# Performance work log

Measured on AMD Instinct MI355X. Metric: run time of the kernel, lower is better.

Reference implementation:

```python
import jax, jax.numpy as jnp
import numpy as np

N_NODES = 50000
N_EDGES = 800000
IN_C, HID_C, OUT_C = 64, 64, 32


def setup_inputs() -> dict:
    key = jax.random.key(0)
    ks = jax.random.split(key, 8)
    x = jax.random.normal(ks[0], (N_NODES, IN_C), dtype=jnp.float32)
    edge_index = jax.random.randint(ks[1], (2, N_EDGES), 0, N_NODES, dtype=jnp.int64)
    s1 = 1.0 / np.sqrt(IN_C)
    s2 = 1.0 / np.sqrt(HID_C)
    W_rel1 = jax.random.uniform(ks[2], (IN_C, HID_C), jnp.float32, -s1, s1)
    W_root1 = jax.random.uniform(ks[3], (IN_C, HID_C), jnp.float32, -s1, s1)
    b1 = jax.random.uniform(ks[4], (HID_C,), jnp.float32, -s1, s1)
    W_rel2 = jax.random.uniform(ks[5], (HID_C, OUT_C), jnp.float32, -s2, s2)
    W_root2 = jax.random.uniform(ks[6], (HID_C, OUT_C), jnp.float32, -s2, s2)
    b2 = jax.random.uniform(ks[7], (OUT_C,), jnp.float32, -s2, s2)
    return {"x": x, "edge_index": edge_index, "W_rel1": W_rel1, "W_root1": W_root1,
            "b1": b1, "W_rel2": W_rel2, "W_root2": W_root2, "b2": b2}


def _graph_conv(x, src, dst, W_rel, W_root, b):
    # aggregate neighbor features (sum over incoming edges), then linear
    agg = jax.ops.segment_sum(x[src], dst, num_segments=N_NODES)  # [N, C_in]
    return agg @ W_rel + x @ W_root + b


def reference(x, edge_index, W_rel1, W_root1, b1, W_rel2, W_root2, b2):
    src, dst = edge_index[0], edge_index[1]
    h = jax.nn.relu(_graph_conv(x, src, dst, W_rel1, W_root1, b1))
    out = _graph_conv(h, src, dst, W_rel2, W_root2, b2)
    return out
```

## Files before the change

kernel.cpp:

```cpp
#include <hip/hip_runtime.h>

static constexpr int N_NODES = 50000;
static constexpr int N_EDGES = 800000;

static constexpr int NBK      = 196;
static constexpr int BCAP     = 5120;
static constexpr int MAXE     = BCAP / 512;
static constexpr int BIN_TILE = 4096;
static constexpr int BIN_BLOCKS = (N_EDGES + BIN_TILE - 1) / BIN_TILE;
static constexpr int PRE1_TILES  = (N_NODES + 15) / 16;
static constexpr int PRE1_BLOCKS = (PRE1_TILES + 3) / 4;

typedef __attribute__((ext_vector_type(8))) short   bf16x8;
typedef __attribute__((ext_vector_type(4))) float   floatx4;

__device__ __forceinline__ unsigned short f2b(float f) {
    union { float f; unsigned u; } v; v.f = f;
    unsigned r = v.u + 0x7FFFu + ((v.u >> 16) & 1u);
    return (unsigned short)(r >> 16);
}
__device__ __forceinline__ float blo(unsigned v) {
    union { unsigned u; float f; } c; c.u = v << 16; return c.f;
}
__device__ __forceinline__ float bhi(unsigned v) {
    union { unsigned u; float f; } c; c.u = v & 0xffff0000u; return c.f;
}
__device__ __forceinline__ unsigned pk2(float a, float b) {
    return (unsigned)f2b(a) | ((unsigned)f2b(b) << 16);
}

__device__ __forceinline__ void bin_body(
    int bb, const int* __restrict__ srcv, const int* __restrict__ dstv,
    int* __restrict__ bcnt, unsigned* __restrict__ epair)
{
    __shared__ unsigned stage[BIN_TILE];
    __shared__ int cnt[256];
    __shared__ int scn[256];
    __shared__ int wtot[4], wbase[4];
    __shared__ int pref[NBK];
    __shared__ int gbase[NBK];

    int tid   = threadIdx.x;
    int lane  = tid & 63;
    int wv    = tid >> 6;
    int base  = bb * BIN_TILE;
    int tileN = min(BIN_TILE, N_EDGES - base);

    cnt[tid] = 0;
    __syncthreads();

    unsigned pk[16]; int sl[16];
#pragma unroll
    for (int j = 0; j < 16; ++j) {
        int i = tid + j * 256;
        pk[j] = 0xFFFFFFFFu; sl[j] = 0;
        if (i < tileN) {
            unsigned s = (unsigned)srcv[base + i];
            unsigned d = (unsigned)dstv[base + i];
            pk[j] = (s << 16) | d;
            sl[j] = atomicAdd(&cnt[d >> 8], 1);
        }
    }
    __syncthreads();

    {
        int v = cnt[tid];
        int orig = v;
        for (int off = 1; off < 64; off <<= 1) {
            int t2 = __shfl_up(v, off);
            if (lane >= off) v += t2;
        }
        scn[tid] = v - orig;
        if (lane == 63) wtot[wv] = v;
    }
    __syncthreads();
    if (tid == 0) {
        int r = 0;
#pragma unroll
        for (int k = 0; k < 4; ++k) { int t2 = wtot[k]; wbase[k] = r; r += t2; }
    }
    __syncthreads();
    if (tid < NBK) {
        pref[tid]  = scn[tid] + wbase[wv];
        gbase[tid] = tid * BCAP + atomicAdd(&bcnt[tid], cnt[tid]);
    }
    __syncthreads();

#pragma unroll
    for (int j = 0; j < 16; ++j) {
        if (pk[j] != 0xFFFFFFFFu) {
            int b = (int)((pk[j] & 0xFFFFu) >> 8);
            stage[pref[b] + sl[j]] = pk[j];
        }
    }
    __syncthreads();

    for (int i = tid; i < tileN; i += 256) {
        unsigned pd = stage[i];
        int b = (int)((pd & 0xFFFFu) >> 8);
        epair[(size_t)gbase[b] + (i - pref[b])] = ((pd >> 16) << 8) | (pd & 255u);
    }
}

__device__ __forceinline__ void pre1_body(
    int bb, const float* __restrict__ x,
    const float* __restrict__ Wrel, const float* __restrict__ Wroot,
    const float* __restrict__ bias,
    unsigned short* __restrict__ u1, unsigned short* __restrict__ r1)
{
    int lane = threadIdx.x & 63;
    int c15  = lane & 15;
    int q    = lane >> 4;

    bf16x8 bf[2][4][2];
#pragma unroll
    for (int mat = 0; mat < 2; ++mat) {
        const float* W = mat ? Wroot : Wrel;
#pragma unroll
        for (int ct = 0; ct < 4; ++ct) {
            int c = ct * 16 + c15;
#pragma unroll
            for (int kf = 0; kf < 2; ++kf) {
                int kb = kf * 32 + q * 8;
                bf16x8 f;
#pragma unroll
                for (int j = 0; j < 8; ++j)
                    f[j] = (short)f2b(W[(kb + j) * 64 + c]);
                bf[mat][ct][kf] = f;
            }
        }
    }
    float bv[4];
#pragma unroll
    for (int ct = 0; ct < 4; ++ct) bv[ct] = bias[ct * 16 + c15];

    int tile = bb * 4 + (threadIdx.x >> 6);
    if (tile * 16 >= N_NODES) return;
    int row0 = tile * 16;

    const float* xr = x + (size_t)(row0 + c15) * 64;
    bf16x8 a0, a1;
#pragma unroll
    for (int j = 0; j < 8; ++j) {
        a0[j] = (short)f2b(xr[q * 8 + j]);
        a1[j] = (short)f2b(xr[32 + q * 8 + j]);
    }

    floatx4 z = {0.f, 0.f, 0.f, 0.f};
    floatx4 acc[2][4];
#pragma unroll
    for (int mat = 0; mat < 2; ++mat)
#pragma unroll
        for (int ct = 0; ct < 4; ++ct) {
            floatx4 a = __builtin_amdgcn_mfma_f32_16x16x32_bf16(a0, bf[mat][ct][0], z, 0, 0, 0);
            acc[mat][ct] = __builtin_amdgcn_mfma_f32_16x16x32_bf16(a1, bf[mat][ct][1], a, 0, 0, 0);
        }

#pragma unroll
    for (int reg = 0; reg < 4; ++reg) {
        int row = row0 + q * 4 + reg;
        uint2 uu, rr;
        uu.x = pk2(acc[0][0][reg],          acc[0][1][reg]);
        uu.y = pk2(acc[0][2][reg],          acc[0][3][reg]);
        rr.x = pk2(acc[1][0][reg] + bv[0],  acc[1][1][reg] + bv[1]);
        rr.y = pk2(acc[1][2][reg] + bv[2],  acc[1][3][reg] + bv[3]);
        *reinterpret_cast<uint2*>(u1 + (size_t)row * 64 + c15 * 4) = uu;
        *reinterpret_cast<uint2*>(r1 + (size_t)row * 64 + c15 * 4) = rr;
    }
}

__global__ __launch_bounds__(256) void k_binpre1(
    const int* __restrict__ srcv, const int* __restrict__ dstv,
    int* __restrict__ bcnt, unsigned* __restrict__ epair,
    const float* __restrict__ x,
    const float* __restrict__ Wrel, const float* __restrict__ Wroot,
    const float* __restrict__ bias,
    unsigned short* __restrict__ u1, unsigned short* __restrict__ r1)
{
    if ((int)blockIdx.x < BIN_BLOCKS)
        bin_body(blockIdx.x, srcv, dstv, bcnt, epair);
    else
        pre1_body(blockIdx.x - BIN_BLOCKS, x, Wrel, Wroot, bias, u1, r1);
}

__global__ __launch_bounds__(512) void k_build(
    const unsigned* __restrict__ epair, const int* __restrict__ bcnt,
    int* __restrict__ offsets, int* __restrict__ esrc)
{
    __shared__ int cnt[256];
    __shared__ int scn[256];
    __shared__ int start[256];
    __shared__ int wtot[4], wbase[4];
    __shared__ int s_base;

    int b = blockIdx.x;
    int t = threadIdx.x;
    int lane = t & 63;
    int node0 = b << 8;
    int ncnt  = min(256, N_NODES - node0);
    int beg   = b * BCAP;
    int m     = bcnt[b];

    if (t < 256) cnt[t] = 0;
    __syncthreads();

    unsigned ev[MAXE]; int sl[MAXE];
#pragma unroll
    for (int j = 0; j < MAXE; ++j) {
        int i = t + j * 512;
        ev[j] = 0; sl[j] = -1;
        if (i < m) {
            ev[j] = epair[beg + i];
            sl[j] = atomicAdd(&cnt[ev[j] & 255u], 1);
        }
    }

    if (t < 64) {
        int pre = 0;
#pragma unroll
        for (int k = 0; k < 4; ++k) {
            int i = t + (k << 6);
            if (i < b) pre += bcnt[i];
        }
        for (int off = 1; off < 64; off <<= 1) pre += __shfl_xor(pre, off);
        if (t == 0) s_base = pre;
    }
    __syncthreads();

    if (t < 256) {
        int v = cnt[t];
        int orig = v;
        for (int off = 1; off < 64; off <<= 1) {
            int t2 = __shfl_up(v, off);
            if (lane >= off) v += t2;
        }
        scn[t] = v - orig;
        if (lane == 63) wtot[t >> 6] = v;
    }
    __syncthreads();
    if (t == 0) {
        int r = 0;
#pragma unroll
        for (int k = 0; k < 4; ++k) { int q = wtot[k]; wbase[k] = r; r += q; }
    }
    __syncthreads();
    if (t < 256) {
        int st = s_base + scn[t] + wbase[t >> 6];
        start[t] = st;
        if (t < ncnt) offsets[node0 + t] = st;
    }
    if (b == 0 && t == 0) offsets[N_NODES] = N_EDGES;
    __syncthreads();

#pragma unroll
    for (int j = 0; j < MAXE; ++j) {
        if (sl[j] >= 0)
            esrc[start[ev[j] & 255u] + sl[j]] = (int)(ev[j] >> 8);
    }
}

__global__ __launch_bounds__(1024) void k_aggf(
    const unsigned short* __restrict__ u1,
    const unsigned short* __restrict__ r1,
    const int* __restrict__ offsets, const int* __restrict__ esrc,
    const float* __restrict__ Wrel,
    const float* __restrict__ Wroot,
    const float* __restrict__ bias,
    unsigned short* __restrict__ u2,
    unsigned short* __restrict__ r2)
{
    __shared__ unsigned short hlds[16 * 64];

    int w    = threadIdx.x >> 6;
    int lane = threadIdx.x & 63;
    int j    = lane & 7;
    int slot = lane >> 3;

    int node = blockIdx.x * 16 + w;
    if (node < N_NODES) {
        int beg = offsets[node], end = offsets[node + 1];
        float s0 = 0.f, s1 = 0.f, s2 = 0.f, s3 = 0.f;
        float s4 = 0.f, s5 = 0.f, s6 = 0.f, s7 = 0.f;
        for (int e = beg + slot; e < end; e += 8) {
            int sv = esrc[e];
            uint4 v = *reinterpret_cast<const uint4*>(u1 + (size_t)sv * 64 + j * 8);
            s0 += blo(v.x); s1 += bhi(v.x);
            s2 += blo(v.y); s3 += bhi(v.y);
            s4 += blo(v.z); s5 += bhi(v.z);
            s6 += blo(v.w); s7 += bhi(v.w);
        }
        s0 += __shfl_xor(s0, 32); s1 += __shfl_xor(s1, 32);
        s2 += __shfl_xor(s2, 32); s3 += __shfl_xor(s3, 32);
        s4 += __shfl_xor(s4, 32); s5 += __shfl_xor(s5, 32);
        s6 += __shfl_xor(s6, 32); s7 += __shfl_xor(s7, 32);
        s0 += __shfl_xor(s0, 16); s1 += __shfl_xor(s1, 16);
        s2 += __shfl_xor(s2, 16); s3 += __shfl_xor(s3, 16);
        s4 += __shfl_xor(s4, 16); s5 += __shfl_xor(s5, 16);
        s6 += __shfl_xor(s6, 16); s7 += __shfl_xor(s7, 16);
        s0 += __shfl_xor(s0, 8);  s1 += __shfl_xor(s1, 8);
        s2 += __shfl_xor(s2, 8);  s3 += __shfl_xor(s3, 8);
        s4 += __shfl_xor(s4, 8);  s5 += __shfl_xor(s5, 8);
        s6 += __shfl_xor(s6, 8);  s7 += __shfl_xor(s7, 8);
        if (lane < 8) {
            uint4 rv = *reinterpret_cast<const uint4*>(r1 + (size_t)node * 64 + j * 8);
            float v0 = fmaxf(s0 + blo(rv.x), 0.f);
            float v1 = fmaxf(s1 + bhi(rv.x), 0.f);
            float v2 = fmaxf(s2 + blo(rv.y), 0.f);
            float v3 = fmaxf(s3 + bhi(rv.y), 0.f);
            float v4 = fmaxf(s4 + blo(rv.z), 0.f);
            float v5 = fmaxf(s5 + bhi(rv.z), 0.f);
            float v6 = fmaxf(s6 + blo(rv.w), 0.f);
            float v7 = fmaxf(s7 + bhi(rv.w), 0.f);
            uint4 o;
            o.x = pk2(v0, v1); o.y = pk2(v2, v3);
            o.z = pk2(v4, v5); o.w = pk2(v6, v7);
            unsigned byte = (unsigned)w * 128u + (((unsigned)j * 16u) ^ (((unsigned)w & 7u) << 4));
            *reinterpret_cast<uint4*>((char*)hlds + byte) = o;
        }
    }
    __syncthreads();

    if (w >= 2) return;
    int row0 = blockIdx.x * 16;
    if (row0 >= N_NODES) return;
    int c15 = lane & 15;
    int q   = lane >> 4;

    const float* W = w ? Wroot : Wrel;
    bf16x8 bf[2][2];
#pragma unroll
    for (int ct = 0; ct < 2; ++ct) {
        int c = ct * 16 + c15;
#pragma unroll
        for (int kf = 0; kf < 2; ++kf) {
            bf16x8 f;
#pragma unroll
            for (int jj = 0; jj < 8; ++jj) {
                int p = kf * 32 + q * 8 + jj;
                int tk = (p & 3) * 16 + (p >> 2);
                f[jj] = (short)f2b(W[tk * 32 + c]);
            }
            bf[ct][kf] = f;
        }
    }
    float bv[2];
#pragma unroll
    for (int ct = 0; ct < 2; ++ct) bv[ct] = w ? bias[ct * 16 + c15] : 0.0f;

    int r = c15;
    unsigned sw = ((unsigned)r & 7u) << 4;
    bf16x8 a0 = *reinterpret_cast<const bf16x8*>((char*)hlds + (unsigned)r * 128u + (((unsigned)q * 16u) ^ sw));
    bf16x8 a1 = *reinterpret_cast<const bf16x8*>((char*)hlds + (unsigned)r * 128u + ((((unsigned)q + 4u) * 16u) ^ sw));

    floatx4 z = {0.f, 0.f, 0.f, 0.f};
    floatx4 acc[2];
#pragma unroll
    for (int ct = 0; ct < 2; ++ct) {
        floatx4 a = __builtin_amdgcn_mfma_f32_16x16x32_bf16(a0, bf[ct][0], z, 0, 0, 0);
        acc[ct] = __builtin_amdgcn_mfma_f32_16x16x32_bf16(a1, bf[ct][1], a, 0, 0, 0);
    }

    unsigned short* dst = w ? r2 : u2;
#pragma unroll
    for (int reg = 0; reg < 4; ++reg) {
        int row = row0 + q * 4 + reg;
        unsigned vv = pk2(acc[0][reg] + bv[0], acc[1][reg] + bv[1]);
        *reinterpret_cast<unsigned*>(dst + (size_t)row * 32 + c15 * 2) = vv;
    }
}

__global__ __launch_bounds__(256) void k_agg32(
    const unsigned short* __restrict__ u2,
    const unsigned short* __restrict__ r2,
    const int* __restrict__ offsets, const int* __restrict__ esrc,
    float* __restrict__ out)
{
    int lane = threadIdx.x & 63;
    int node = (blockIdx.x * blockDim.x + threadIdx.x) >> 6;
    if (node >= N_NODES) return;
    int j    = lane & 3;
    int slot = lane >> 2;
    int beg = offsets[node], end = offsets[node + 1];
    float s0 = 0.f, s1 = 0.f, s2 = 0.f, s3 = 0.f;
    float s4 = 0.f, s5 = 0.f, s6 = 0.f, s7 = 0.f;
    for (int e = beg + slot; e < end; e += 16) {
        int sv = esrc[e];
        uint4 v = *reinterpret_cast<const uint4*>(u2 + (size_t)sv * 32 + j * 8);
        s0 += blo(v.x); s1 += bhi(v.x);
        s2 += blo(v.y); s3 += bhi(v.y);
        s4 += blo(v.z); s5 += bhi(v.z);
        s6 += blo(v.w); s7 += bhi(v.w);
    }
    s0 += __shfl_xor(s0, 32); s1 += __shfl_xor(s1, 32);
    s2 += __shfl_xor(s2, 32); s3 += __shfl_xor(s3, 32);
    s4 += __shfl_xor(s4, 32); s5 += __shfl_xor(s5, 32);
    s6 += __shfl_xor(s6, 32); s7 += __shfl_xor(s7, 32);
    s0 += __shfl_xor(s0, 16); s1 += __shfl_xor(s1, 16);
    s2 += __shfl_xor(s2, 16); s3 += __shfl_xor(s3, 16);
    s4 += __shfl_xor(s4, 16); s5 += __shfl_xor(s5, 16);
    s6 += __shfl_xor(s6, 16); s7 += __shfl_xor(s7, 16);
    s0 += __shfl_xor(s0, 8);  s1 += __shfl_xor(s1, 8);
    s2 += __shfl_xor(s2, 8);  s3 += __shfl_xor(s3, 8);
    s4 += __shfl_xor(s4, 8);  s5 += __shfl_xor(s5, 8);
    s6 += __shfl_xor(s6, 8);  s7 += __shfl_xor(s7, 8);
    s0 += __shfl_xor(s0, 4);  s1 += __shfl_xor(s1, 4);
    s2 += __shfl_xor(s2, 4);  s3 += __shfl_xor(s3, 4);
    s4 += __shfl_xor(s4, 4);  s5 += __shfl_xor(s5, 4);
    s6 += __shfl_xor(s6, 4);  s7 += __shfl_xor(s7, 4);
    if (lane < 4) {
        uint4 rv = *reinterpret_cast<const uint4*>(r2 + (size_t)node * 32 + j * 8);
        float4 oA, oB;
        oA.x = s0 + blo(rv.x);  oB.x = s1 + bhi(rv.x);
        oA.y = s2 + blo(rv.y);  oB.y = s3 + bhi(rv.y);
        oA.z = s4 + blo(rv.z);  oB.z = s5 + bhi(rv.z);
        oA.w = s6 + blo(rv.w);  oB.w = s7 + bhi(rv.w);
        *reinterpret_cast<float4*>(out + (size_t)node * 32 + j * 4)      = oA;
        *reinterpret_cast<float4*>(out + (size_t)node * 32 + 16 + j * 4) = oB;
    }
}

extern "C" void kernel_launch(void* const* d_in, const int* in_sizes, int n_in,
                              void* d_out, int out_size, void* d_ws, size_t ws_size,
                              hipStream_t stream) {
    const float* x      = (const float*)d_in[0];
    const int*   ei     = (const int*)  d_in[1];
    const float* Wrel1  = (const float*)d_in[2];
    const float* Wroot1 = (const float*)d_in[3];
    const float* b1     = (const float*)d_in[4];
    const float* Wrel2  = (const float*)d_in[5];
    const float* Wroot2 = (const float*)d_in[6];
    const float* b2     = (const float*)d_in[7];
    float*       out    = (float*)d_out;

    const int* srcv = ei;
    const int* dstv = ei + N_EDGES;

    char* p = (char*)d_ws;
    auto alloc = [&](size_t bytes) {
        char* r = p;
        p += (bytes + 255) & ~(size_t)255;
        return r;
    };
    int*      offsets = (int*)     alloc(sizeof(int) * (N_NODES + 1));
    int*      bcnt    = (int*)     alloc(sizeof(int) * NBK);
    unsigned* epair   = (unsigned*)alloc(sizeof(unsigned) * (size_t)NBK * BCAP);
    int*      esrc    = (int*)     alloc(sizeof(int) * N_EDGES);
    unsigned short* u1 = (unsigned short*)alloc(sizeof(short) * (size_t)N_NODES * 64);
    unsigned short* r1 = (unsigned short*)alloc(sizeof(short) * (size_t)N_NODES * 64);
    unsigned short* u2 = (unsigned short*)alloc(sizeof(short) * (size_t)N_NODES * 32);
    unsigned short* r2 = (unsigned short*)alloc(sizeof(short) * (size_t)N_NODES * 32);

    const int nodeBlocks = (N_NODES * 64 + 255) / 256;
    const int aggfBlocks = (N_NODES + 15) / 16;

    hipMemsetAsync(bcnt, 0, sizeof(int) * NBK, stream);
    k_binpre1<<<BIN_BLOCKS + PRE1_BLOCKS, 256, 0, stream>>>(
        srcv, dstv, bcnt, epair, x, Wrel1, Wroot1, b1, u1, r1);
    k_build<<<NBK, 512, 0, stream>>>(epair, bcnt, offsets, esrc);

    k_aggf<<<aggfBlocks, 1024, 0, stream>>>(u1, r1, offsets, esrc,
                                            Wrel2, Wroot2, b2, u2, r2);

    k_agg32<<<nodeBlocks, 256, 0, stream>>>(u2, r2, offsets, esrc, out);
}
```

Before: 86.45 us.

## Split layer-1 dense transform across bin and build kernels to balance load

Splits the layer-1 node-transform blocks (MFMA x·W) into two halves: one still fused with edge binning, the other fused into the CSR build kernel. The build kernel now runs with 256 threads per block instead of 512, holding twice as many edges per thread in registers. The aim is to fill idle CUs during the small build launch and shorten the binning launch. In exchange, the build phase carries more register pressure per thread and longer serial loops.

```diff
diff --git a/kernel.cpp b/kernel.cpp
--- a/kernel.cpp
+++ b/kernel.cpp
@@ -5,11 +5,12 @@
 
 static constexpr int NBK      = 196;
 static constexpr int BCAP     = 5120;
-static constexpr int MAXE     = BCAP / 512;
+static constexpr int MAXE     = BCAP / 256;
 static constexpr int BIN_TILE = 4096;
 static constexpr int BIN_BLOCKS = (N_EDGES + BIN_TILE - 1) / BIN_TILE;
-static constexpr int PRE1_TILES  = (N_NODES + 15) / 16;
-static constexpr int PRE1_BLOCKS = (PRE1_TILES + 3) / 4;
+static constexpr int PRE1_TILES = (N_NODES + 15) / 16;
+static constexpr int PRE1_SPLIT = 391;
+static constexpr int PRE1_REST  = 391;
 
 typedef __attribute__((ext_vector_type(8))) short   bf16x8;
 typedef __attribute__((ext_vector_type(4))) float   floatx4;
@@ -103,7 +104,7 @@
 }
 
 __device__ __forceinline__ void pre1_body(
-    int bb, const float* __restrict__ x,
+    int tile, const float* __restrict__ x,
     const float* __restrict__ Wrel, const float* __restrict__ Wroot,
     const float* __restrict__ bias,
     unsigned short* __restrict__ u1, unsigned short* __restrict__ r1)
@@ -134,7 +135,6 @@
 #pragma unroll
     for (int ct = 0; ct < 4; ++ct) bv[ct] = bias[ct * 16 + c15];
 
-    int tile = bb * 4 + (threadIdx.x >> 6);
     if (tile * 16 >= N_NODES) return;
     int row0 = tile * 16;
 
@@ -169,6 +169,81 @@
     }
 }
 
+__device__ __forceinline__ void build_body(
+    int b, const unsigned* __restrict__ epair, const int* __restrict__ bcnt,
+    int* __restrict__ offsets, int* __restrict__ esrc)
+{
+    __shared__ int cnt[256];
+    __shared__ int scn[256];
+    __shared__ int start[256];
+    __shared__ int wtot[4], wbase[4];
+    __shared__ int s_base;
+
+    int t = threadIdx.x;
+    int lane = t & 63;
+    int node0 = b << 8;
+    int ncnt  = min(256, N_NODES - node0);
+    int beg   = b * BCAP;
+    int m     = bcnt[b];
+
+    cnt[t] = 0;
+    __syncthreads();
+
+    unsigned ev[MAXE]; int sl[MAXE];
+#pragma unroll
+    for (int j = 0; j < MAXE; ++j) {
+        int i = t + j * 256;
+        ev[j] = 0; sl[j] = -1;
+        if (i < m) {
+            ev[j] = epair[beg + i];
+            sl[j] = atomicAdd(&cnt[ev[j] & 255u], 1);
+        }
+    }
+
+    if (t < 64) {
+        int pre = 0;
+#pragma unroll
+        for (int k = 0; k < 4; ++k) {
+            int i = t + (k << 6);
+            if (i < b) pre += bcnt[i];
+        }
+        for (int off = 1; off < 64; off <<= 1) pre += __shfl_xor(pre, off);
+        if (t == 0) s_base = pre;
+    }
+    __syncthreads();
+
+    {
+        int v = cnt[t];
+        int orig = v;
+        for (int off = 1; off < 64; off <<= 1) {
+            int t2 = __shfl_up(v, off);
+            if (lane >= off) v += t2;
+        }
+        scn[t] = v - orig;
+        if (lane == 63) wtot[t >> 6] = v;
+    }
+    __syncthreads();
+    if (t == 0) {
+        int r = 0;
+#pragma unroll
+        for (int k = 0; k < 4; ++k) { int q = wtot[k]; wbase[k] = r; r += q; }
+    }
+    __syncthreads();
+    {
+        int st = s_base + scn[t] + wbase[t >> 6];
+        start[t] = st;
+        if (t < ncnt) offsets[node0 + t] = st;
+    }
+    if (b == 0 && t == 0) offsets[N_NODES] = N_EDGES;
+    __syncthreads();
+
+#pragma unroll
+    for (int j = 0; j < MAXE; ++j) {
+        if (sl[j] >= 0)
+            esrc[start[ev[j] & 255u] + sl[j]] = (int)(ev[j] >> 8);
+    }
+}
+
 __global__ __launch_bounds__(256) void k_binpre1(
     const int* __restrict__ srcv, const int* __restrict__ dstv,
     int* __restrict__ bcnt, unsigned* __restrict__ epair,
@@ -180,83 +255,23 @@
     if ((int)blockIdx.x < BIN_BLOCKS)
         bin_body(blockIdx.x, srcv, dstv, bcnt, epair);
     else
-        pre1_body(blockIdx.x - BIN_BLOCKS, x, Wrel, Wroot, bias, u1, r1);
-}
-
-__global__ __launch_bounds__(512) void k_build(
+        pre1_body((blockIdx.x - BIN_BLOCKS) * 4 + (threadIdx.x >> 6),
+                  x, Wrel, Wroot, bias, u1, r1);
+}
+
+__global__ __launch_bounds__(256) void k_buildpre1(
     const unsigned* __restrict__ epair, const int* __restrict__ bcnt,
-    int* __restrict__ offsets, int* __restrict__ esrc)
-{
-    __shared__ int cnt[256];
-    __shared__ int scn[256];
-    __shared__ int start[256];
-    __shared__ int wtot[4], wbase[4];
-    __shared__ int s_base;
-
-    int b = blockIdx.x;
-    int t = threadIdx.x;
-    int lane = t & 63;
-    int node0 = b << 8;
-    int ncnt  = min(256, N_NODES - node0);
-    int beg   = b * BCAP;
-    int m     = bcnt[b];
-
-    if (t < 256) cnt[t] = 0;
-    __syncthreads();
-
-    unsigned ev[MAXE]; int sl[MAXE];
-#pragma unroll
-    for (int j = 0; j < MAXE; ++j) {
-        int i = t + j * 512;
-        ev[j] = 0; sl[j] = -1;
-        if (i < m) {
-            ev[j] = epair[beg + i];
-            sl[j] = atomicAdd(&cnt[ev[j] & 255u], 1);
-        }
-    }
-
-    if (t < 64) {
-        int pre = 0;
-#pragma unroll
-        for (int k = 0; k < 4; ++k) {
-            int i = t + (k << 6);
-            if (i < b) pre += bcnt[i];
-        }
-        for (int off = 1; off < 64; off <<= 1) pre += __shfl_xor(pre, off);
-        if (t == 0) s_base = pre;
-    }
-    __syncthreads();
-
-    if (t < 256) {
-        int v = cnt[t];
-        int orig = v;
-        for (int off = 1; off < 64; off <<= 1) {
-            int t2 = __shfl_up(v, off);
-            if (lane >= off) v += t2;
-        }
-        scn[t] = v - orig;
-        if (lane == 63) wtot[t >> 6] = v;
-    }
-    __syncthreads();
-    if (t == 0) {
-        int r = 0;
-#pragma unroll
-        for (int k = 0; k < 4; ++k) { int q = wtot[k]; wbase[k] = r; r += q; }
-    }
-    __syncthreads();
-    if (t < 256) {
-        int st = s_base + scn[t] + wbase[t >> 6];
-        start[t] = st;
-        if (t < ncnt) offsets[node0 + t] = st;
-    }
-    if (b == 0 && t == 0) offsets[N_NODES] = N_EDGES;
-    __syncthreads();
-
-#pragma unroll
-    for (int j = 0; j < MAXE; ++j) {
-        if (sl[j] >= 0)
-            esrc[start[ev[j] & 255u] + sl[j]] = (int)(ev[j] >> 8);
-    }
+    int* __restrict__ offsets, int* __restrict__ esrc,
+    const float* __restrict__ x,
+    const float* __restrict__ Wrel, const float* __restrict__ Wroot,
+    const float* __restrict__ bias,
+    unsigned short* __restrict__ u1, unsigned short* __restrict__ r1)
+{
+    if ((int)blockIdx.x < NBK)
+        build_body(blockIdx.x, epair, bcnt, offsets, esrc);
+    else
+        pre1_body(PRE1_SPLIT * 4 + (blockIdx.x - NBK) * 4 + (threadIdx.x >> 6),
+                  x, Wrel, Wroot, bias, u1, r1);
 }
 
 __global__ __launch_bounds__(1024) void k_aggf(
@@ -454,9 +469,12 @@
     const int aggfBlocks = (N_NODES + 15) / 16;
 
     hipMemsetAsync(bcnt, 0, sizeof(int) * NBK, stream);
-    k_binpre1<<<BIN_BLOCKS + PRE1_BLOCKS, 256, 0, stream>>>(
+
+    k_binpre1<<<BIN_BLOCKS + PRE1_SPLIT, 256, 0, stream>>>(
         srcv, dstv, bcnt, epair, x, Wrel1, Wroot1, b1, u1, r1);
-    k_build<<<NBK, 512, 0, stream>>>(epair, bcnt, offsets, esrc);
+
+    k_buildpre1<<<NBK + PRE1_REST, 256, 0, stream>>>(
+        epair, bcnt, offsets, esrc, x, Wrel1, Wroot1, b1, u1, r1);
 
     k_aggf<<<aggfBlocks, 1024, 0, stream>>>(u1, r1, offsets, esrc,
                                             Wrel2, Wroot2, b2, u2, r2);
```

Measured after the change: 88.79 us. +2.7%, slower.
